# Kernel optimization log

Hardware: AMD Instinct MI355X
Metric: run time of the kernel (lower is better)

Reference implementation:

```python
import jax, jax.numpy as jnp
import numpy as np

REGION_NUM = 16
B, C, H, W = 16, 3, 512, 512


def setup_inputs() -> dict:
    key = jax.random.key(0)
    k1, k2 = jax.random.split(key)
    x = jax.random.normal(k1, (B, C, H, W), dtype=jnp.float32)
    # torch.rand(total_splits) hoisted out of forward for determinism:
    # shape (b*c, region_num - 1)
    rand_perc = jax.random.uniform(k2, (B * C, REGION_NUM - 1), dtype=jnp.float32)
    return {"x": x, "rand_perc": rand_perc}


def reference(x, rand_perc):
    b, c, h, w = x.shape
    bc = b * c
    x_flat = x.reshape(bc, h, w)                       # (bc, h, w)

    flat = x_flat.reshape(bc, -1)
    min_val = flat.min(axis=1)                         # (bc,)
    max_val = flat.max(axis=1)                         # (bc,)

    # region boundaries: unsorted random splits, as in the original
    splits = rand_perc * (max_val - min_val)[:, None] + min_val[:, None]  # (bc, R-1)
    left = jnp.concatenate([min_val[:, None], splits], axis=1)            # (bc, R)
    right = jnpp if False else jnp.concatenate([splits, (max_val + 1e-6)[:, None]], axis=1)  # (bc, R)

    # per-pixel region mask, argmax picks first matching region
    x_exp = x_flat[:, None, :, :]                      # (bc, 1, h, w)
    mask = (x_exp >= left[:, :, None, None]) & (x_exp < right[:, :, None, None])  # (bc, R, h, w)
    idx = jnp.argmax(mask, axis=1)                     # (bc, h, w)

    # gather lower boundary per pixel
    quant = jnp.take_along_axis(left, idx.reshape(bc, -1), axis=1).reshape(bc, h, w)
    return quant.reshape(b, c, h, w)
```

## Files before the change

kernel.cpp:

```cpp
#include <hip/hip_runtime.h>
#include <math.h>

#define IMGS 48
#define IMG_ELEMS (512*512)
#define BLOCKS_A_PER_IMG 64
#define BLOCKS_C_PER_IMG 256

__global__ __launch_bounds__(256) void minmax_kernel(const float* __restrict__ x,
                                                     float* __restrict__ pmin,
                                                     float* __restrict__ pmax) {
    int blk = blockIdx.x;
    int img = blk >> 6;
    int b   = blk & 63;
    const float4* xin = (const float4*)x + (size_t)img * (IMG_ELEMS / 4) + (size_t)b * 1024;
    int t = threadIdx.x;

    float mn = INFINITY, mx = -INFINITY;
#pragma unroll
    for (int k = 0; k < 4; ++k) {
        float4 d = xin[k * 256 + t];
        mn = fminf(mn, fminf(fminf(d.x, d.y), fminf(d.z, d.w)));
        mx = fmaxf(mx, fmaxf(fmaxf(d.x, d.y), fmaxf(d.z, d.w)));
    }
#pragma unroll
    for (int off = 32; off >= 1; off >>= 1) {
        mn = fminf(mn, __shfl_xor(mn, off));
        mx = fmaxf(mx, __shfl_xor(mx, off));
    }
    __shared__ float smn[4], smx[4];
    int wave = t >> 6;
    if ((t & 63) == 0) { smn[wave] = mn; smx[wave] = mx; }
    __syncthreads();
    if (t == 0) {
        mn = fminf(fminf(smn[0], smn[1]), fminf(smn[2], smn[3]));
        mx = fmaxf(fmaxf(smx[0], smx[1]), fmaxf(smx[2], smx[3]));
        pmin[blk] = mn;
        pmax[blk] = mx;
    }
}

__global__ __launch_bounds__(64) void bounds_kernel(const float* __restrict__ pmin,
                                                    const float* __restrict__ pmax,
                                                    const float* __restrict__ rp,
                                                    float* __restrict__ wsb,
                                                    float* __restrict__ wv) {
    int img  = blockIdx.x;
    int lane = threadIdx.x;

    float mn = pmin[img * 64 + lane];
    float mx = pmax[img * 64 + lane];
#pragma unroll
    for (int off = 32; off >= 1; off >>= 1) {
        mn = fminf(mn, __shfl_xor(mn, off));
        mx = fmaxf(mx, __shfl_xor(mx, off));
    }

    __shared__ float sb[17];
    __shared__ float L[16], R[16];
    float maxeps = mx + 1e-6f;
    if (lane < 15) {
        float s = __fadd_rn(__fmul_rn(rp[img * 15 + lane], __fsub_rn(mx, mn)), mn);
        sb[1 + lane] = s;
        L[1 + lane]  = s;
        R[lane]      = s;
    }
    if (lane == 0) {
        sb[0] = mn; sb[16] = maxeps;
        L[0]  = mn; R[15]  = maxeps;
    }
    __syncthreads();
    if (lane == 0) {
        for (int i = 1; i < 17; ++i) {
            float key = sb[i];
            int j = i - 1;
            while (j >= 0 && sb[j] > key) { sb[j + 1] = sb[j]; --j; }
            sb[j + 1] = key;
        }
    }
    __syncthreads();
    if (lane < 16) {
        float t = sb[lane];
        float v = L[0];
        bool found = false;
#pragma unroll
        for (int r = 0; r < 16; ++r) {
            bool c = (t >= L[r]) && (t < R[r]);
            if (c && !found) { v = L[r]; found = true; }
        }
        wv[img * 16 + lane] = v;
        if (lane >= 1) wsb[img * 16 + (lane - 1)] = sb[lane];
    }
}

__global__ __launch_bounds__(256) void quant_kernel(const float* __restrict__ x,
                                                    const float* __restrict__ wsb,
                                                    const float* __restrict__ wv,
                                                    float* __restrict__ out) {
    int blk = blockIdx.x;
    int img = __builtin_amdgcn_readfirstlane(blk >> 8);
    const float* SBp = wsb + img * 16;
    const float* Vp  = wv  + img * 16;

    float sb[15], vv[16];
#pragma unroll
    for (int k = 0; k < 15; ++k) sb[k] = SBp[k];
#pragma unroll
    for (int k = 0; k < 16; ++k) vv[k] = Vp[k];

    size_t f4 = (size_t)blk * 256 + threadIdx.x;
    float4 d = ((const float4*)x)[f4];

    float ox = vv[0], oy = vv[0], oz = vv[0], ow = vv[0];
#pragma unroll
    for (int k = 1; k < 16; ++k) {
        ox = (d.x >= sb[k - 1]) ? vv[k] : ox;
        oy = (d.y >= sb[k - 1]) ? vv[k] : oy;
        oz = (d.z >= sb[k - 1]) ? vv[k] : oz;
        ow = (d.w >= sb[k - 1]) ? vv[k] : ow;
    }
    float4 o = make_float4(ox, oy, oz, ow);
    ((float4*)out)[f4] = o;
}

extern "C" void kernel_launch(void* const* d_in, const int* in_sizes, int n_in,
                              void* d_out, int out_size, void* d_ws, size_t ws_size,
                              hipStream_t stream) {
    const float* x  = (const float*)d_in[0];
    const float* rp = (const float*)d_in[1];
    float* out = (float*)d_out;
    float* ws  = (float*)d_ws;

    float* pmin = ws;
    float* pmax = ws + 3072;
    float* wsb  = ws + 6144;
    float* wv   = ws + 6912;

    minmax_kernel<<<IMGS * BLOCKS_A_PER_IMG, 256, 0, stream>>>(x, pmin, pmax);
    bounds_kernel<<<IMGS, 64, 0, stream>>>(pmin, pmax, rp, wsb, wv);
    quant_kernel<<<IMGS * BLOCKS_C_PER_IMG, 256, 0, stream>>>(x, wsb, wv, out);
}
```

Before: 114.1 us.

## Fuse bounds computation into quantize kernel with shuffle-based rank sort

Drops the separate single-wave bounds kernel. Each quantize block now recomputes the per-image boundaries: it reduces the 64 partial min/max values, sorts the 17 boundaries by rank counting with wave shuffles, and derives each region's value. The quantize grid shrinks to 64 blocks per image, with each thread handling four float4s and issuing its loads before the bounds work so they can overlap. This removes one kernel launch and its serialization gap, but every block repeats the small bounds computation and the grid has fewer, larger blocks.

Result: faster. 110.9 us (-2.8%).

```diff
diff --git a/kernel.cpp b/kernel.cpp
--- a/kernel.cpp
+++ b/kernel.cpp
@@ -4,7 +4,7 @@
 #define IMGS 48
 #define IMG_ELEMS (512*512)
 #define BLOCKS_A_PER_IMG 64
-#define BLOCKS_C_PER_IMG 256
+#define BLOCKS_C_PER_IMG 64
 
 __global__ __launch_bounds__(256) void minmax_kernel(const float* __restrict__ x,
                                                      float* __restrict__ pmin,
@@ -32,94 +32,92 @@
     if ((t & 63) == 0) { smn[wave] = mn; smx[wave] = mx; }
     __syncthreads();
     if (t == 0) {
-        mn = fminf(fminf(smn[0], smn[1]), fminf(smn[2], smn[3]));
-        mx = fmaxf(fmaxf(smx[0], smx[1]), fmaxf(smx[2], smx[3]));
-        pmin[blk] = mn;
-        pmax[blk] = mx;
+        pmin[blk] = fminf(fminf(smn[0], smn[1]), fminf(smn[2], smn[3]));
+        pmax[blk] = fmaxf(fmaxf(smx[0], smx[1]), fmaxf(smx[2], smx[3]));
     }
 }
 
-__global__ __launch_bounds__(64) void bounds_kernel(const float* __restrict__ pmin,
-                                                    const float* __restrict__ pmax,
-                                                    const float* __restrict__ rp,
-                                                    float* __restrict__ wsb,
-                                                    float* __restrict__ wv) {
-    int img  = blockIdx.x;
-    int lane = threadIdx.x;
+__global__ __launch_bounds__(256) void quant_fused(const float* __restrict__ x,
+                                                   const float* __restrict__ pmin,
+                                                   const float* __restrict__ pmax,
+                                                   const float* __restrict__ rp,
+                                                   float* __restrict__ out) {
+    int blk  = blockIdx.x;
+    int img  = blk >> 6;
+    int b    = blk & 63;
+    int t    = threadIdx.x;
+    int lane = t & 63;
+    int wave = t >> 6;
 
-    float mn = pmin[img * 64 + lane];
-    float mx = pmax[img * 64 + lane];
+    __shared__ float sorted[17];
+    __shared__ float s_sb[15], s_vv[16];
+
+    size_t base = (size_t)img * (IMG_ELEMS / 4) + (size_t)b * 1024 + t;
+    const float4* xin = (const float4*)x + base;
+    float4 d0 = xin[0];
+    float4 d1 = xin[256];
+    float4 d2 = xin[512];
+    float4 d3 = xin[768];
+
+    if (wave == 0) {
+        float mn = pmin[img * 64 + lane];
+        float mx = pmax[img * 64 + lane];
 #pragma unroll
-    for (int off = 32; off >= 1; off >>= 1) {
-        mn = fminf(mn, __shfl_xor(mn, off));
-        mx = fmaxf(mx, __shfl_xor(mx, off));
-    }
+        for (int off = 32; off >= 1; off >>= 1) {
+            mn = fminf(mn, __shfl_xor(mn, off));
+            mx = fmaxf(mx, __shfl_xor(mx, off));
+        }
+        float maxeps = __fadd_rn(mx, 1e-6f);
 
-    __shared__ float sb[17];
-    __shared__ float L[16], R[16];
-    float maxeps = mx + 1e-6f;
-    if (lane < 15) {
-        float s = __fadd_rn(__fmul_rn(rp[img * 15 + lane], __fsub_rn(mx, mn)), mn);
-        sb[1 + lane] = s;
-        L[1 + lane]  = s;
-        R[lane]      = s;
-    }
-    if (lane == 0) {
-        sb[0] = mn; sb[16] = maxeps;
-        L[0]  = mn; R[15]  = maxeps;
-    }
-    __syncthreads();
-    if (lane == 0) {
-        for (int i = 1; i < 17; ++i) {
-            float key = sb[i];
-            int j = i - 1;
-            while (j >= 0 && sb[j] > key) { sb[j + 1] = sb[j]; --j; }
-            sb[j + 1] = key;
+        float u = (lane >= 1 && lane <= 15) ? rp[img * 15 + (lane - 1)] : 0.0f;
+        float split = __fadd_rn(__fmul_rn(u, __fsub_rn(mx, mn)), mn);
+        float bval  = (lane == 0) ? mn : (lane == 16 ? maxeps : split);
+
+        int rank = 0;
+#pragma unroll
+        for (int i = 0; i < 17; ++i) {
+            float vi = __shfl(bval, i);
+            rank += (vi < bval) || (vi == bval && i < lane);
         }
-    }
-    __syncthreads();
-    if (lane < 16) {
-        float t = sb[lane];
-        float v = L[0];
+        if (lane < 17) sorted[rank] = bval;
+
+        float tg = sorted[lane & 15];
+        float v  = __shfl(bval, 0);
         bool found = false;
 #pragma unroll
         for (int r = 0; r < 16; ++r) {
-            bool c = (t >= L[r]) && (t < R[r]);
-            if (c && !found) { v = L[r]; found = true; }
+            float Lr = __shfl(bval, r);
+            float Rr = __shfl(bval, r + 1);
+            bool c = (tg >= Lr) && (tg < Rr);
+            v = (c && !found) ? Lr : v;
+            found = found || c;
         }
-        wv[img * 16 + lane] = v;
-        if (lane >= 1) wsb[img * 16 + (lane - 1)] = sb[lane];
+        if (lane < 16)  s_vv[lane] = v;
+        if (lane < 15)  s_sb[lane] = sorted[lane + 1];
     }
-}
-
-__global__ __launch_bounds__(256) void quant_kernel(const float* __restrict__ x,
-                                                    const float* __restrict__ wsb,
-                                                    const float* __restrict__ wv,
-                                                    float* __restrict__ out) {
-    int blk = blockIdx.x;
-    int img = __builtin_amdgcn_readfirstlane(blk >> 8);
-    const float* SBp = wsb + img * 16;
-    const float* Vp  = wv  + img * 16;
+    __syncthreads();
 
     float sb[15], vv[16];
 #pragma unroll
-    for (int k = 0; k < 15; ++k) sb[k] = SBp[k];
+    for (int k = 0; k < 15; ++k) sb[k] = s_sb[k];
 #pragma unroll
-    for (int k = 0; k < 16; ++k) vv[k] = Vp[k];
+    for (int k = 0; k < 16; ++k) vv[k] = s_vv[k];
 
-    size_t f4 = (size_t)blk * 256 + threadIdx.x;
-    float4 d = ((const float4*)x)[f4];
-
-    float ox = vv[0], oy = vv[0], oz = vv[0], ow = vv[0];
+    float4* oput = (float4*)out + base;
+    float4 din[4] = {d0, d1, d2, d3};
 #pragma unroll
-    for (int k = 1; k < 16; ++k) {
-        ox = (d.x >= sb[k - 1]) ? vv[k] : ox;
-        oy = (d.y >= sb[k - 1]) ? vv[k] : oy;
-        oz = (d.z >= sb[k - 1]) ? vv[k] : oz;
-        ow = (d.w >= sb[k - 1]) ? vv[k] : ow;
+    for (int k = 0; k < 4; ++k) {
+        float4 d = din[k];
+        float ox = vv[0], oy = vv[0], oz = vv[0], ow = vv[0];
+#pragma unroll
+        for (int j = 1; j < 16; ++j) {
+            ox = (d.x >= sb[j - 1]) ? vv[j] : ox;
+            oy = (d.y >= sb[j - 1]) ? vv[j] : oy;
+            oz = (d.z >= sb[j - 1]) ? vv[j] : oz;
+            ow = (d.w >= sb[j - 1]) ? vv[j] : ow;
+        }
+        oput[k * 256] = make_float4(ox, oy, oz, ow);
     }
-    float4 o = make_float4(ox, oy, oz, ow);
-    ((float4*)out)[f4] = o;
 }
 
 extern "C" void kernel_launch(void* const* d_in, const int* in_sizes, int n_in,
@@ -132,10 +130,7 @@
 
     float* pmin = ws;
     float* pmax = ws + 3072;
-    float* wsb  = ws + 6144;
-    float* wv   = ws + 6912;
 
     minmax_kernel<<<IMGS * BLOCKS_A_PER_IMG, 256, 0, stream>>>(x, pmin, pmax);
-    bounds_kernel<<<IMGS, 64, 0, stream>>>(pmin, pmax, rp, wsb, wv);
-    quant_kernel<<<IMGS * BLOCKS_C_PER_IMG, 256, 0, stream>>>(x, wsb, wv, out);
+    quant_fused<<<IMGS * BLOCKS_C_PER_IMG, 256, 0, stream>>>(x, pmin, pmax, rp, out);
 }
```
